# Optimization experiments

Measured on AMD Instinct MI355X. Metric: run time of the kernel, lower is better.

The kernel has to match this reference:

```python
import jax, jax.numpy as jnp
import numpy as np

N = 10000      # nodes
E = 160000     # edges (before self-loops)
H = 8          # heads
D_IN, D_H1, D_H2 = 165, 128, 1    # per-head channels of gat1 / gat2
HID = H * D_H1                    # 1024


def batchnorm(x, gamma, beta, eps=1e-5):
    # training-mode BatchNorm1d: biased batch statistics over the node axis
    mu = x.mean(0)
    var = x.var(0)
    return (x - mu) * jax.lax.rsqrt(var + eps) * gamma + beta


def gatv2(x, src, dst, Wl, bl, Wr, br, att, bias, heads, out_ch, concat, n_nodes):
    # PyG GATv2Conv: lin_l on source, lin_r on target; e = att . LeakyReLU(xl_j + xr_i)
    xl = (x @ Wl + bl).reshape(n_nodes, heads, out_ch)   # source transform
    xr = (x @ Wr + br).reshape(n_nodes, heads, out_ch)   # target transform
    e = jax.nn.leaky_relu(xl[src] + xr[dst], 0.2)        # [E,H,C]
    logits = jnp.einsum('ehc,hc->eh', e, att)            # [E,H]
    # segment softmax over incoming edges of each destination node
    m = jax.lax.stop_gradient(jax.ops.segment_max(logits, dst, num_segments=n_nodes))
    a = jnp.exp(logits - m[dst])
    s = jax.ops.segment_sum(a, dst, num_segments=n_nodes)
    alpha = a / (s[dst] + 1e-16)                          # [E,H]
    out = jax.ops.segment_sum(xl[src] * alpha[..., None], dst, num_segments=n_nodes)
    out = out.reshape(n_nodes, heads * out_ch) if concat else out.mean(1)
    return out + bias


def setup_inputs() -> dict:
    key = jax.random.key(0)
    ks = jax.random.split(key, 12)
    g = lambda k, shape, fan_in: jax.random.normal(k, shape, jnp.float32) * (1.0 / np.sqrt(fan_in))
    return {
        'x': jax.random.normal(ks[0], (N, D_IN), jnp.float32),
        'gamma1': jnp.ones((D_IN,), jnp.float32),
        'beta1': jnp.zeros((D_IN,), jnp.float32),
        'Wl1': g(ks[1], (D_IN, HID), D_IN),
        'bl1': jnp.zeros((HID,), jnp.float32),
        'Wr1': g(ks[2], (D_IN, HID), D_IN),
        'br1': jnp.zeros((HID,), jnp.float32),
        'att1': g(ks[3], (H, D_H1), D_H1),
        'bias1': jnp.zeros((HID,), jnp.float32),
        'gamma2': jnp.ones((HID,), jnp.float32),
        'beta2': jnp.zeros((HID,), jnp.float32),
        'Wl2': g(ks[4], (HID, H * D_H2), HID),
        'bl2': jnp.zeros((H * D_H2,), jnp.float32),
        'Wr2': g(ks[5], (HID, H * D_H2), HID),
        'br2': jnp.zeros((H * D_H2,), jnp.float32),
        'att2': g(ks[6], (H, D_H2), D_H2),
        'bias2': jnp.zeros((D_H2,), jnp.float32),
        'edge_index': jax.random.randint(ks[7], (2, E), 0, N, jnp.int64 if jax.config.jax_enable_x64 else jnp.int32),
    }


def reference(x, gamma1, beta1, Wl1, bl1, Wr1, br1, att1, bias1,
              gamma2, beta2, Wl2, bl2, Wr2, br2, att2, bias2, edge_index):
    loops = jnp.arange(N, dtype=edge_index.dtype)
    src = jnp.concatenate([edge_index[0], loops])   # add_self_loops=True (PyG default)
    dst = jnp.concatenate([edge_index[1], loops])
    h = batchnorm(x, gamma1, beta1)
    h = gatv2(h, src, dst, Wl1, bl1, Wr1, br1, att1, bias1, H, D_H1, True, N)
    h = batchnorm(h, gamma2, beta2)
    h = jax.nn.leaky_relu(h, 0.01)                  # F.leaky_relu default slope
    out = gatv2(h, src, dst, Wl2, bl2, Wr2, br2, att2, bias2, H, D_H2, False, N)
    return out
```

## Files before the change

kernel.cpp:

```cpp
#include <hip/hip_runtime.h>

#define NN   10000
#define E0   160000
#define ET   170000
#define DIN  165
#define KP   192
#define HID  1024
#define NH   8
#define AP   200
#define CP   136
#define K2P  1032
#define BNROW 64
#define BNBLK 157


typedef __bf16 bf16x8 __attribute__((ext_vector_type(8)));
typedef float  f32x4  __attribute__((ext_vector_type(4)));
typedef float  f32x2  __attribute__((ext_vector_type(2)));

__device__ __forceinline__ float bf2f(unsigned short u) {
    unsigned int i = ((unsigned int)u) << 16;
    return __builtin_bit_cast(float, i);
}
__device__ __forceinline__ unsigned short f2bf(float f) {
    unsigned int i = __builtin_bit_cast(unsigned int, f);
    i += 0x7fffu + ((i >> 16) & 1u);
    return (unsigned short)(i >> 16);
}
__device__ __forceinline__ float fin(float x) {
    return fminf(fmaxf(x, -1e30f), 1e30f);
}
__device__ __forceinline__ int clampi(int s) {
    return min(max(s, 0), NN - 1);
}
__device__ __forceinline__ void unpack8(uint4 u, float* f) {
    f[0]=bf2f((unsigned short)(u.x)); f[1]=bf2f((unsigned short)(u.x>>16));
    f[2]=bf2f((unsigned short)(u.y)); f[3]=bf2f((unsigned short)(u.y>>16));
    f[4]=bf2f((unsigned short)(u.z)); f[5]=bf2f((unsigned short)(u.z>>16));
    f[6]=bf2f((unsigned short)(u.w)); f[7]=bf2f((unsigned short)(u.w>>16));
}
__device__ __forceinline__ f32x2 up2(unsigned int u) {
    f32x2 r;
    r.x = __builtin_bit_cast(float, u << 16);
    r.y = __builtin_bit_cast(float, u & 0xffff0000u);
    return r;
}

__global__ __launch_bounds__(256) void debug_fill(float* __restrict__ out, float val) {
    int i = blockIdx.x * 256 + threadIdx.x;
    if (i < NN) out[i] = val;
}

__global__ __launch_bounds__(256) void fuseA_kernel(const float* __restrict__ x,
                                                    float* __restrict__ colsum, float* __restrict__ colsq,
                                                    const int* __restrict__ ei, int* __restrict__ deg) {
    __shared__ float xs[BNROW * DIN];
    const int b = blockIdx.x;
    const int tid = threadIdx.x;
    if (b < BNBLK) {
        const int r0 = b * BNROW;
        const int nrows = min(BNROW, NN - r0);
        const int total = nrows * DIN;
        const float2* src = (const float2*)(x + (size_t)r0 * DIN);
        float2* dstl = (float2*)xs;
        for (int idx = tid; idx < (total >> 1); idx += 256)
            dstl[idx] = src[idx];
        __syncthreads();
        const int c = tid;
        if (c >= DIN) return;
        float a0=0,a1=0,a2=0,a3=0, q0=0,q1=0,q2=0,q3=0;
        int r = 0;
        for (; r + 3 < nrows; r += 4) {
            float v0 = xs[(r    ) * DIN + c];
            float v1 = xs[(r + 1) * DIN + c];
            float v2 = xs[(r + 2) * DIN + c];
            float v3 = xs[(r + 3) * DIN + c];
            a0 += v0; q0 += v0 * v0;
            a1 += v1; q1 += v1 * v1;
            a2 += v2; q2 += v2 * v2;
            a3 += v3; q3 += v3 * v3;
        }
        for (; r < nrows; ++r) {
            float v = xs[r * DIN + c];
            a0 += v; q0 += v * v;
        }
        atomicAdd(&colsum[c], (a0 + a1) + (a2 + a3));
        atomicAdd(&colsq[c],  (q0 + q1) + (q2 + q3));
    } else {
        int e = (b - BNBLK) * 256 + tid;
        if (e >= ET) return;
        int d = (e < E0) ? ei[E0 + e] : (e - E0);
        atomicAdd(&deg[clampi(d)], 1);
    }
}

__global__ __launch_bounds__(1024) void fuseB_kernel(
    const int* __restrict__ deg,
    int* __restrict__ offs, int* __restrict__ cur, int* __restrict__ perm,
    const float* __restrict__ x,
    const float* __restrict__ colsum, const float* __restrict__ colsq,
    const float* __restrict__ gamma, const float* __restrict__ beta,
    unsigned short* __restrict__ hn) {
    if (blockIdx.x != 0) {
        int idx = (blockIdx.x - 1) * 1024 + threadIdx.x;
        if (idx >= NN * KP) return;
        int r = idx / KP, c = idx - r * KP;
        float v = 0.f;
        if (c < DIN) {
            float mu  = colsum[c] * (1.f / NN);
            float var = fmaxf(colsq[c] * (1.f / NN) - mu * mu, 0.f);
            float a = gamma[c] * rsqrtf(var + 1e-5f);
            float b = beta[c] - mu * a;
            v = fin(x[(size_t)r * DIN + c] * a + b);
        }
        hn[idx] = f2bf(v);
        return;
    }
    __shared__ int wsum[16];
    __shared__ int bins[64];
    __shared__ int bcur[64];
    const int tid = threadIdx.x;
    const int base = tid * 10;
    int loc[10];
    int run = 0;
    #pragma unroll
    for (int j = 0; j < 10; ++j) {
        int idx = base + j;
        int v = (idx < NN) ? deg[idx] : 0;
        loc[j] = run;
        run += v;
    }
    const int lane = tid & 63;
    const int w = tid >> 6;
    int inc = run;
    #pragma unroll
    for (int s = 1; s < 64; s <<= 1) {
        int t = __shfl_up(inc, s);
        if (lane >= s) inc += t;
    }
    if (lane == 63) wsum[w] = inc;
    if (tid < 64) bins[tid] = 0;
    __syncthreads();
    int woff = 0;
    #pragma unroll
    for (int k = 0; k < 16; ++k) woff += (k < w) ? wsum[k] : 0;
    const int toff = woff + inc - run;
    #pragma unroll
    for (int j = 0; j < 10; ++j) {
        int idx = base + j;
        if (idx < NN) {
            int e = toff + loc[j]; offs[idx] = e; cur[idx] = e;
            atomicAdd(&bins[63 - min(deg[idx], 63)], 1);
        }
    }
    if (tid == 1023) offs[NN] = woff + inc;
    __syncthreads();
    if (tid < 64) {
        int v = bins[tid];
        int binc = v;
        #pragma unroll
        for (int s = 1; s < 64; s <<= 1) {
            int t = __shfl_up(binc, s);
            if (tid >= s) binc += t;
        }
        bcur[tid] = binc - v;
    }
    __syncthreads();
    #pragma unroll
    for (int j = 0; j < 10; ++j) {
        int idx = base + j;
        if (idx < NN) {
            int pos = atomicAdd(&bcur[63 - min(deg[idx], 63)], 1);
            perm[pos] = idx;
        }
    }
}

__global__ __launch_bounds__(256) void fuseC_kernel(const float* __restrict__ wl,
                                                    const float* __restrict__ wr,
                                                    unsigned short* __restrict__ wlt,
                                                    unsigned short* __restrict__ wrt,
                                                    const int* __restrict__ ei,
                                                    int* __restrict__ cur, int* __restrict__ ssrc) {
    const int b = blockIdx.x;
    if (b < 192) {
        const int z  = b / 96;
        const int rm = b - z * 96;
        const int ky = rm / 6;
        const int kx = rm - ky * 6;
        const float* src    = z ? wr  : wl;
        unsigned short* dst = z ? wrt : wlt;
        __shared__ float ts[32][65];
        const int k0 = kx * 32;
        const int n0 = ky * 64;
        const int tid = threadIdx.x;
        for (int idx = tid; idx < 32 * 64; idx += 256) {
            int k = idx >> 6, n = idx & 63;
            ts[k][n] = (k0 + k < DIN) ? src[(size_t)(k0 + k) * HID + n0 + n] : 0.f;
        }
        __syncthreads();
        for (int idx = tid; idx < 64 * 32; idx += 256) {
            int n = idx >> 5, k = idx & 31;
            dst[(size_t)(n0 + n) * KP + k0 + k] = f2bf(ts[k][n]);
        }
    } else {
        int e = (b - 192) * 256 + threadIdx.x;
        if (e >= ET) return;
        int s, d;
        if (e < E0) { s = ei[e]; d = ei[E0 + e]; }
        else        { s = e - E0; d = e - E0; }
        int pos = atomicAdd(&cur[clampi(d)], 1);
        if (pos >= 0 && pos < ET) ssrc[pos] = clampi(s);
    }
}

__global__ __launch_bounds__(256) void gemm1_kernel(
    const unsigned short* __restrict__ hn,
    const unsigned short* __restrict__ wlt,
    const unsigned short* __restrict__ wrt,
    const float* __restrict__ bl,
    const float* __restrict__ br,
    unsigned short* __restrict__ xl,
    unsigned short* __restrict__ xr) {
    __shared__ unsigned short as[64 * AP];
    const int tid  = threadIdx.x;
    const int lane = tid & 63;
    const int wave = tid >> 6;
    const int col  = lane & 15;
    const int q    = lane >> 4;

    const int m0 = blockIdx.x * 64;
    const int z  = blockIdx.y >> 3;
    const int nb = (blockIdx.y & 7) * 128;
    const unsigned short* wt = z ? wrt : wlt;

    bf16x8 B[2][6];
    {
        const int bc0 = nb + wave * 32 + col;
        #pragma unroll
        for (int nt = 0; nt < 2; ++nt) {
            const unsigned short* wp = wt + (size_t)(bc0 + nt * 16) * KP + q * 8;
            #pragma unroll
            for (int kt = 0; kt < 6; ++kt)
                B[nt][kt] = __builtin_bit_cast(bf16x8, *(const uint4*)(wp + kt * 32));
        }
    }

    {
        const int r  = tid >> 2;
        const int s0 = (tid & 3) * 48;
        const int grow = m0 + r;
        uint4 t0 = {0,0,0,0}, t1 = t0, t2 = t0, t3 = t0, t4 = t0, t5 = t0;
        if (grow < NN) {
            const unsigned short* gp = hn + (size_t)grow * KP + s0;
            t0 = *(const uint4*)(gp);
            t1 = *(const uint4*)(gp + 8);
            t2 = *(const uint4*)(gp + 16);
            t3 = *(const uint4*)(gp + 24);
            t4 = *(const uint4*)(gp + 32);
            t5 = *(const uint4*)(gp + 40);
        }
        unsigned short* lp = as + r * AP + s0;
        *(uint4*)(lp)      = t0;
        *(uint4*)(lp + 8)  = t1;
        *(uint4*)(lp + 16) = t2;
        *(uint4*)(lp + 24) = t3;
        *(uint4*)(lp + 32) = t4;
        *(uint4*)(lp + 40) = t5;
    }
    __syncthreads();

    f32x4 acc[4][2];
    #pragma unroll
    for (int mi = 0; mi < 4; ++mi)
        for (int nt = 0; nt < 2; ++nt)
            acc[mi][nt][0] = acc[mi][nt][1] = acc[mi][nt][2] = acc[mi][nt][3] = 0.f;

    #pragma unroll
    for (int kt = 0; kt < 6; ++kt) {
        const int kk = kt * 32 + q * 8;
        bf16x8 A[4];
        #pragma unroll
        for (int mi = 0; mi < 4; ++mi)
            A[mi] = __builtin_bit_cast(bf16x8, *(const uint4*)(as + (mi * 16 + col) * AP + kk));
        #pragma unroll
        for (int mi = 0; mi < 4; ++mi) {
            acc[mi][0] = __builtin_amdgcn_mfma_f32_16x16x32_bf16(A[mi], B[0][kt], acc[mi][0], 0, 0, 0);
            acc[mi][1] = __builtin_amdgcn_mfma_f32_16x16x32_bf16(A[mi], B[1][kt], acc[mi][1], 0, 0, 0);
        }
    }

    __syncthreads();
    #pragma unroll
    for (int nt = 0; nt < 2; ++nt) {
        const int lc = wave * 32 + nt * 16 + col;
        const float bv = (z ? br : bl)[nb + lc];
        #pragma unroll
        for (int mi = 0; mi < 4; ++mi) {
            #pragma unroll
            for (int r = 0; r < 4; ++r) {
                const int lr = mi * 16 + q * 4 + r;
                as[lr * CP + lc] = f2bf(fin(acc[mi][nt][r] + bv));
            }
        }
    }
    __syncthreads();
    {
        const int r  = tid >> 2;
        const int sg = (tid & 3) * 32;
        const int grow = m0 + r;
        if (grow < NN) {
            unsigned short* dst = (z ? xr : xl) + (size_t)grow * HID + nb + sg;
            const unsigned short* sp = as + r * CP + sg;
            *(uint4*)(dst)      = *(const uint4*)(sp);
            *(uint4*)(dst + 8)  = *(const uint4*)(sp + 8);
            *(uint4*)(dst + 16) = *(const uint4*)(sp + 16);
            *(uint4*)(dst + 24) = *(const uint4*)(sp + 24);
        }
    }
}

__global__ __launch_bounds__(256) void gat1_node(
    const unsigned short* __restrict__ xl1, const unsigned short* xr1,
    const float* __restrict__ att1, const float* __restrict__ bias1,
    const int* __restrict__ offs, const int* __restrict__ ssrc,
    const int* __restrict__ perm,
    unsigned short* agg) {
    const int lane = threadIdx.x & 63;
    const int wave = threadIdx.x >> 6;
    const int i = perm[blockIdx.x * 4 + wave];
    const int e0 = offs[i];
    const int e1 = max(offs[i + 1], e0);

    f32x2 xr2[8], at2[8], o2[8];
    {
        const uint4* xp = (const uint4*)(xr1 + (size_t)i * HID + lane * 16);
        uint4 u0 = xp[0], u1 = xp[1];
        unsigned int w[8] = {u0.x, u0.y, u0.z, u0.w, u1.x, u1.y, u1.z, u1.w};
        const float4* ap = (const float4*)(att1 + lane * 16);
        float4 a0 = ap[0], a1 = ap[1], a2 = ap[2], a3 = ap[3];
        float af[16] = {a0.x,a0.y,a0.z,a0.w, a1.x,a1.y,a1.z,a1.w,
                        a2.x,a2.y,a2.z,a2.w, a3.x,a3.y,a3.z,a3.w};
        #pragma unroll
        for (int j = 0; j < 8; ++j) {
            xr2[j] = up2(w[j]);
            at2[j].x = af[2*j]; at2[j].y = af[2*j+1];
            o2[j].x = 0.f; o2[j].y = 0.f;
        }
    }
    float s = 0.f;

    int e = e0;
    for (; e + 1 < e1; e += 2) {
        const int s0i = clampi(ssrc[e]);
        const int s1i = clampi(ssrc[e + 1]);
        const uint4* xp0 = (const uint4*)(xl1 + (size_t)s0i * HID + lane * 16);
        const uint4* xp1 = (const uint4*)(xl1 + (size_t)s1i * HID + lane * 16);
        uint4 a0 = xp0[0], a1 = xp0[1], b0 = xp1[0], b1 = xp1[1];
        unsigned int wa[8] = {a0.x,a0.y,a0.z,a0.w, a1.x,a1.y,a1.z,a1.w};
        unsigned int wb[8] = {b0.x,b0.y,b0.z,b0.w, b1.x,b1.y,b1.z,b1.w};
        f32x2 xa[8], xb[8];
        #pragma unroll
        for (int j = 0; j < 8; ++j) { xa[j] = up2(wa[j]); xb[j] = up2(wb[j]); }
        f32x2 pa = {0.f, 0.f}, pb = {0.f, 0.f};
        #pragma unroll
        for (int j = 0; j < 8; ++j) {
            f32x2 va = xa[j] + xr2[j];
            f32x2 vb = xb[j] + xr2[j];
            va = __builtin_elementwise_max(va, 0.2f * va);
            vb = __builtin_elementwise_max(vb, 0.2f * vb);
            pa = __builtin_elementwise_fma(at2[j], va, pa);
            pb = __builtin_elementwise_fma(at2[j], vb, pb);
        }
        float p0 = pa.x + pa.y;
        float p1 = pb.x + pb.y;
        p0 += __shfl_xor(p0, 1); p0 += __shfl_xor(p0, 2); p0 += __shfl_xor(p0, 4);
        p1 += __shfl_xor(p1, 1); p1 += __shfl_xor(p1, 2); p1 += __shfl_xor(p1, 4);
        const float aa0 = __expf(fminf(fin(p0), 50.f));
        const float aa1 = __expf(fminf(fin(p1), 50.f));
        s += aa0 + aa1;
        f32x2 av0; av0.x = aa0; av0.y = aa0;
        f32x2 av1; av1.x = aa1; av1.y = aa1;
        #pragma unroll
        for (int j = 0; j < 8; ++j)
            o2[j] = __builtin_elementwise_fma(av0, xa[j],
                    __builtin_elementwise_fma(av1, xb[j], o2[j]));
    }
    if (e < e1) {
        const int sidx = clampi(ssrc[e]);
        const uint4* xp = (const uint4*)(xl1 + (size_t)sidx * HID + lane * 16);
        uint4 u0 = xp[0], u1 = xp[1];
        unsigned int w[8] = {u0.x,u0.y,u0.z,u0.w, u1.x,u1.y,u1.z,u1.w};
        f32x2 xv[8];
        #pragma unroll
        for (int j = 0; j < 8; ++j) xv[j] = up2(w[j]);
        f32x2 p2 = {0.f, 0.f};
        #pragma unroll
        for (int j = 0; j < 8; ++j) {
            f32x2 v = xv[j] + xr2[j];
            v = __builtin_elementwise_max(v, 0.2f * v);
            p2 = __builtin_elementwise_fma(at2[j], v, p2);
        }
        float p = p2.x + p2.y;
        p += __shfl_xor(p, 1); p += __shfl_xor(p, 2); p += __shfl_xor(p, 4);
        const float a = __expf(fminf(fin(p), 50.f));
        s += a;
        f32x2 av; av.x = a; av.y = a;
        #pragma unroll
        for (int j = 0; j < 8; ++j)
            o2[j] = __builtin_elementwise_fma(av, xv[j], o2[j]);
    }

    const float inv = 1.f / (s + 1e-16f);
    const float4* bp = (const float4*)(bias1 + lane * 16);
    float4 b0 = bp[0], b1 = bp[1], b2 = bp[2], b3 = bp[3];
    float bb[16] = {b0.x,b0.y,b0.z,b0.w, b1.x,b1.y,b1.z,b1.w,
                    b2.x,b2.y,b2.z,b2.w, b3.x,b3.y,b3.z,b3.w};
    unsigned short ov[16];
    #pragma unroll
    for (int j = 0; j < 8; ++j) {
        ov[2*j]   = f2bf(fin(o2[j].x * inv + bb[2*j]));
        ov[2*j+1] = f2bf(fin(o2[j].y * inv + bb[2*j+1]));
    }
    uint4* op = (uint4*)(agg + (size_t)i * HID + lane * 16);
    op[0] = *(const uint4*)&ov[0];
    op[1] = *(const uint4*)&ov[8];
}

__global__ __launch_bounds__(256) void bn2_stats(const unsigned short* __restrict__ agg,
                                                 float* __restrict__ colsum, float* __restrict__ colsq) {
    __shared__ float mrg[128 * 16];
    const int tid  = threadIdx.x;
    const int half = tid >> 7;
    const int cc   = (tid & 127) * 8;
    const int r0   = blockIdx.x * 80 + half;
    float s[8], q[8];
    #pragma unroll
    for (int j = 0; j < 8; ++j) { s[j] = 0.f; q[j] = 0.f; }
    #pragma unroll 4
    for (int rr = 0; rr < 40; ++rr) {
        const int r = r0 + rr * 2;
        uint4 u = *(const uint4*)(agg + (size_t)r * HID + cc);
        float v[8];
        unpack8(u, v);
        #pragma unroll
        for (int j = 0; j < 8; ++j) { s[j] += v[j]; q[j] += v[j] * v[j]; }
    }
    if (half) {
        float* m = &mrg[(tid & 127) * 16];
        #pragma unroll
        for (int j = 0; j < 8; ++j) { m[j] = s[j]; m[8 + j] = q[j]; }
    }
    __syncthreads();
    if (!half) {
        const float* m = &mrg[tid * 16];
        #pragma unroll
        for (int j = 0; j < 8; ++j) {
            atomicAdd(&colsum[cc + j], s[j] + m[j]);
            atomicAdd(&colsq[cc + j],  q[j] + m[8 + j]);
        }
    }
}

__global__ __launch_bounds__(256) void gemm2_kernel(
    const unsigned short* __restrict__ agg,
    const float* __restrict__ colsum, const float* __restrict__ colsq,
    const float* __restrict__ gamma, const float* __restrict__ beta,
    const float* __restrict__ wl2, const float* __restrict__ wr2,
    const float* __restrict__ bl2, const float* __restrict__ br2,
    float* __restrict__ xl2, float* __restrict__ xr2) {
    __shared__ unsigned short bs[16 * K2P];
    __shared__ float a2s[HID], b2s[HID];
    __shared__ float red[4 * 64 * 4];
    const int tid  = threadIdx.x;
    const int lane = tid & 63;
    const int wave = tid >> 6;
    const int col  = lane & 15;
    const int q    = lane >> 4;

    for (int idx = tid; idx < 16 * HID; idx += 256) {
        int n = idx >> 10, k = idx & (HID - 1);
        float v = (n < 8) ? wl2[k * 8 + n] : wr2[k * 8 + (n - 8)];
        bs[n * K2P + k] = f2bf(v);
    }
    for (int cc = tid; cc < HID; cc += 256) {
        float mu  = colsum[cc] * (1.f / NN);
        float var = fmaxf(colsq[cc] * (1.f / NN) - mu * mu, 0.f);
        float a = gamma[cc] * rsqrtf(var + 1e-5f);
        a2s[cc] = a; b2s[cc] = beta[cc] - mu * a;
    }
    __syncthreads();

    const int m0 = blockIdx.x * 16;
    const int am = m0 + col;

    uint4 u[8];
    #pragma unroll
    for (int t = 0; t < 8; ++t) {
        const int kk = (wave * 8 + t) * 32 + q * 8;
        u[t] = *(const uint4*)(agg + (size_t)am * HID + kk);
    }

    f32x4 acc;
    acc[0] = acc[1] = acc[2] = acc[3] = 0.f;
    #pragma unroll
    for (int t = 0; t < 8; ++t) {
        const int kk = (wave * 8 + t) * 32 + q * 8;
        float xv[8];
        unpack8(u[t], xv);
        unsigned short hv[8];
        #pragma unroll
        for (int j = 0; j < 8; ++j) {
            float v = xv[j] * a2s[kk + j] + b2s[kk + j];
            v = fmaxf(v, 0.01f * v);
            hv[j] = f2bf(fin(v));
        }
        bf16x8 af = __builtin_bit_cast(bf16x8, *(const uint4*)hv);
        bf16x8 bf = __builtin_bit_cast(bf16x8, *(const uint4*)&bs[col * K2P + kk]);
        acc = __builtin_amdgcn_mfma_f32_16x16x32_bf16(af, bf, acc, 0, 0, 0);
    }

    *(f32x4*)&red[(wave * 64 + lane) * 4] = acc;
    __syncthreads();
    if (wave == 0) {
        f32x4 a0 = *(const f32x4*)&red[lane * 4];
        f32x4 a1 = *(const f32x4*)&red[(64 + lane) * 4];
        f32x4 a2 = *(const f32x4*)&red[(128 + lane) * 4];
        f32x4 a3 = *(const f32x4*)&red[(192 + lane) * 4];
        acc = (a0 + a1) + (a2 + a3);
        const float bv = (col < 8) ? bl2[col] : br2[col - 8];
        float* outp = (col < 8) ? (xl2 + col) : (xr2 + (col - 8));
        #pragma unroll
        for (int r = 0; r < 4; ++r) {
            const int row = m0 + q * 4 + r;
            outp[row * 8] = fin(acc[r] + bv);
        }
    }
}

__global__ __launch_bounds__(256) void gat2_node(
    const float* __restrict__ xl2, const float* __restrict__ xr2,
    const float* __restrict__ att2, const float* __restrict__ bias2,
    const int* __restrict__ offs, const int* __restrict__ ssrc,
    const int* __restrict__ perm,
    float* __restrict__ out) {
    const int lane = threadIdx.x & 63;
    const int wave = threadIdx.x >> 6;
    const int i = perm[blockIdx.x * 4 + wave];
    const int h = lane & 7, slot = lane >> 3;
    const int e0 = offs[i];
    const int e1 = max(offs[i + 1], e0);
    const float xr_h = xr2[i * 8 + h];
    const float att_h = att2[h];
    float ssum = 0.f, wsum = 0.f;
    for (int eb = e0; eb < e1; eb += 8) {
        int e = eb + slot;
        if (e < e1) {
            float xlv = xl2[clampi(ssrc[e]) * 8 + h];
            float v = xlv + xr_h;
            v = fmaxf(v, 0.2f * v);
            float a = __expf(fminf(fin(att_h * v), 50.f));
            ssum += a; wsum += a * xlv;
        }
    }
    ssum += __shfl_xor(ssum, 8); ssum += __shfl_xor(ssum, 16); ssum += __shfl_xor(ssum, 32);
    wsum += __shfl_xor(wsum, 8); wsum += __shfl_xor(wsum, 16); wsum += __shfl_xor(wsum, 32);
    float v = fin(wsum / (ssum + 1e-16f));
    v += __shfl_xor(v, 1); v += __shfl_xor(v, 2); v += __shfl_xor(v, 4);
    if (lane == 0) out[i] = fin(v * 0.125f + bias2[0]);
}

extern "C" void kernel_launch(void* const* d_in, const int* in_sizes, int n_in,
                              void* d_out, int out_size, void* d_ws, size_t ws_size,
                              hipStream_t stream) {
    float* out = (float*)d_out;

    static const int expected[18] = {
        NN * DIN, DIN, DIN, DIN * HID, HID, DIN * HID, HID, HID, HID,
        HID, HID, HID * NH, NH, HID * NH, NH, NH, 1, 2 * E0
    };
    if (n_in != 18) {
        debug_fill<<<(NN + 255) / 256, 256, 0, stream>>>(out, 8192.f + 64.f * (float)n_in);
        return;
    }
    for (int i = 0; i < 18; ++i) {
        if (in_sizes[i] != expected[i]) {
            debug_fill<<<(NN + 255) / 256, 256, 0, stream>>>(out, 4096.f + 32.f * (float)i);
            return;
        }
    }

    const float* x      = (const float*)d_in[0];
    const float* gamma1 = (const float*)d_in[1];
    const float* beta1  = (const float*)d_in[2];
    const float* Wl1    = (const float*)d_in[3];
    const float* bl1    = (const float*)d_in[4];
    const float* Wr1    = (const float*)d_in[5];
    const float* br1    = (const float*)d_in[6];
    const float* att1   = (const float*)d_in[7];
    const float* bias1  = (const float*)d_in[8];
    const float* gamma2 = (const float*)d_in[9];
    const float* beta2  = (const float*)d_in[10];
    const float* Wl2    = (const float*)d_in[11];
    const float* bl2    = (const float*)d_in[12];
    const float* Wr2    = (const float*)d_in[13];
    const float* br2    = (const float*)d_in[14];
    const float* att2   = (const float*)d_in[15];
    const float* bias2  = (const float*)d_in[16];
    const int*   ei     = (const int*)d_in[17];

    char* p = (char*)d_ws;
    auto alloc = [&](size_t bytes) -> void* {
        void* r = (void*)p;
        p += (bytes + 255) & ~(size_t)255;
        return r;
    };
    unsigned short* xl1  = (unsigned short*)alloc((size_t)NN * HID * 2);
    unsigned short* xr1  = (unsigned short*)alloc((size_t)NN * HID * 2);
    unsigned short* agg  = xr1;
    unsigned short* hn   = (unsigned short*)alloc((size_t)NN * KP * 2);
    unsigned short* wlt  = (unsigned short*)alloc((size_t)HID * KP * 2);
    unsigned short* wrt  = (unsigned short*)alloc((size_t)HID * KP * 2);
    float*          xl2  = (float*)alloc((size_t)NN * 8 * 4);
    float*          xr2  = (float*)alloc((size_t)NN * 8 * 4);
    int*            offs = (int*)alloc((NN + 1) * 4);
    int*            cur  = (int*)alloc(NN * 4);
    int*            ssrc = (int*)alloc(ET * 4);
    int*            perm = (int*)alloc(NN * 4);
    char* zbase = p;
    float* colsum1 = (float*)alloc(DIN * 4);
    float* colsq1  = (float*)alloc(DIN * 4);
    float* colsum2 = (float*)alloc(HID * 4);
    float* colsq2  = (float*)alloc(HID * 4);
    int*   deg     = (int*)alloc(NN * 4);
    size_t zlen = (size_t)(p - zbase);
    hipMemsetAsync(zbase, 0, zlen, stream);

    fuseA_kernel<<<BNBLK + (ET + 255) / 256, 256, 0, stream>>>(x, colsum1, colsq1, ei, deg);
    fuseB_kernel<<<1 + (NN * KP + 1023) / 1024, 1024, 0, stream>>>(
        deg, offs, cur, perm, x, colsum1, colsq1, gamma1, beta1, hn);
    fuseC_kernel<<<192 + (ET + 255) / 256, 256, 0, stream>>>(Wl1, Wr1, wlt, wrt, ei, cur, ssrc);
    gemm1_kernel<<<dim3((NN + 63) / 64, 16), 256, 0, stream>>>(hn, wlt, wrt, bl1, br1, xl1, xr1);
    gat1_node<<<NN / 4, 256, 0, stream>>>(xl1, xr1, att1, bias1, offs, ssrc, perm, agg);
    bn2_stats<<<125, 256, 0, stream>>>(agg, colsum2, colsq2);
    gemm2_kernel<<<NN / 16, 256, 0, stream>>>(agg, colsum2, colsq2, gamma2, beta2,
                                              Wl2, Wr2, bl2, br2, xl2, xr2);
    gat2_node<<<NN / 4, 256, 0, stream>>>(xl2, xr2, att2, bias2, offs, ssrc, perm, out);
}
```

Baseline: 280.8 us.

## Split gat1 aggregation across channel quarters and edge halves per wave

Each destination node's GATv2 aggregation is now spread across four blocks, each handling a 256-channel quarter, and the wave's two 32-lane halves process alternating edges before combining their partial sums with a cross-half shuffle. The grid grows fourfold and each lane holds 8 channels instead of 16. This aims to raise parallelism and occupancy and to shorten the serial edge loop on the dominant gather kernel. The cost is extra index loads and repeated setup across blocks, a wider shuffle reduction, and half-filled lanes at the tail of odd-degree nodes.

```diff
diff --git a/kernel.cpp b/kernel.cpp
--- a/kernel.cpp
+++ b/kernel.cpp
@@ -326,105 +326,78 @@
     const int* __restrict__ offs, const int* __restrict__ ssrc,
     const int* __restrict__ perm,
     unsigned short* agg) {
-    const int lane = threadIdx.x & 63;
-    const int wave = threadIdx.x >> 6;
-    const int i = perm[blockIdx.x * 4 + wave];
+    const int lane    = threadIdx.x & 63;
+    const int wv      = threadIdx.x >> 6;
+    const int quarter = blockIdx.x & 3;
+    const int ngrp    = blockIdx.x >> 2;
+    const int i  = perm[ngrp * 4 + wv];
     const int e0 = offs[i];
-    const int e1 = max(offs[i + 1], e0);
-
-    f32x2 xr2[8], at2[8], o2[8];
+    const int e1 = max(offs[i + 1], e0 + 1);
+    const int cl    = lane & 31;
+    const int halfB = lane >> 5;
+    const int choff = quarter * 256 + cl * 8;
+
+    f32x2 xr2[4], at2[4], o2[4];
     {
-        const uint4* xp = (const uint4*)(xr1 + (size_t)i * HID + lane * 16);
-        uint4 u0 = xp[0], u1 = xp[1];
-        unsigned int w[8] = {u0.x, u0.y, u0.z, u0.w, u1.x, u1.y, u1.z, u1.w};
-        const float4* ap = (const float4*)(att1 + lane * 16);
-        float4 a0 = ap[0], a1 = ap[1], a2 = ap[2], a3 = ap[3];
-        float af[16] = {a0.x,a0.y,a0.z,a0.w, a1.x,a1.y,a1.z,a1.w,
-                        a2.x,a2.y,a2.z,a2.w, a3.x,a3.y,a3.z,a3.w};
-        #pragma unroll
-        for (int j = 0; j < 8; ++j) {
-            xr2[j] = up2(w[j]);
-            at2[j].x = af[2*j]; at2[j].y = af[2*j+1];
-            o2[j].x = 0.f; o2[j].y = 0.f;
-        }
+        uint4 u = *(const uint4*)(xr1 + (size_t)i * HID + choff);
+        xr2[0] = up2(u.x); xr2[1] = up2(u.y); xr2[2] = up2(u.z); xr2[3] = up2(u.w);
+        float4 a0 = *(const float4*)(att1 + choff);
+        float4 a1 = *(const float4*)(att1 + choff + 4);
+        at2[0].x = a0.x; at2[0].y = a0.y; at2[1].x = a0.z; at2[1].y = a0.w;
+        at2[2].x = a1.x; at2[2].y = a1.y; at2[3].x = a1.z; at2[3].y = a1.w;
+        #pragma unroll
+        for (int j = 0; j < 4; ++j) { o2[j].x = 0.f; o2[j].y = 0.f; }
     }
     float s = 0.f;
 
-    int e = e0;
-    for (; e + 1 < e1; e += 2) {
-        const int s0i = clampi(ssrc[e]);
-        const int s1i = clampi(ssrc[e + 1]);
-        const uint4* xp0 = (const uint4*)(xl1 + (size_t)s0i * HID + lane * 16);
-        const uint4* xp1 = (const uint4*)(xl1 + (size_t)s1i * HID + lane * 16);
-        uint4 a0 = xp0[0], a1 = xp0[1], b0 = xp1[0], b1 = xp1[1];
-        unsigned int wa[8] = {a0.x,a0.y,a0.z,a0.w, a1.x,a1.y,a1.z,a1.w};
-        unsigned int wb[8] = {b0.x,b0.y,b0.z,b0.w, b1.x,b1.y,b1.z,b1.w};
-        f32x2 xa[8], xb[8];
-        #pragma unroll
-        for (int j = 0; j < 8; ++j) { xa[j] = up2(wa[j]); xb[j] = up2(wb[j]); }
-        f32x2 pa = {0.f, 0.f}, pb = {0.f, 0.f};
-        #pragma unroll
-        for (int j = 0; j < 8; ++j) {
-            f32x2 va = xa[j] + xr2[j];
-            f32x2 vb = xb[j] + xr2[j];
-            va = __builtin_elementwise_max(va, 0.2f * va);
-            vb = __builtin_elementwise_max(vb, 0.2f * vb);
-            pa = __builtin_elementwise_fma(at2[j], va, pa);
-            pb = __builtin_elementwise_fma(at2[j], vb, pb);
-        }
-        float p0 = pa.x + pa.y;
-        float p1 = pb.x + pb.y;
-        p0 += __shfl_xor(p0, 1); p0 += __shfl_xor(p0, 2); p0 += __shfl_xor(p0, 4);
-        p1 += __shfl_xor(p1, 1); p1 += __shfl_xor(p1, 2); p1 += __shfl_xor(p1, 4);
-        const float aa0 = __expf(fminf(fin(p0), 50.f));
-        const float aa1 = __expf(fminf(fin(p1), 50.f));
-        s += aa0 + aa1;
-        f32x2 av0; av0.x = aa0; av0.y = aa0;
-        f32x2 av1; av1.x = aa1; av1.y = aa1;
-        #pragma unroll
-        for (int j = 0; j < 8; ++j)
-            o2[j] = __builtin_elementwise_fma(av0, xa[j],
-                    __builtin_elementwise_fma(av1, xb[j], o2[j]));
-    }
-    if (e < e1) {
-        const int sidx = clampi(ssrc[e]);
-        const uint4* xp = (const uint4*)(xl1 + (size_t)sidx * HID + lane * 16);
-        uint4 u0 = xp[0], u1 = xp[1];
-        unsigned int w[8] = {u0.x,u0.y,u0.z,u0.w, u1.x,u1.y,u1.z,u1.w};
-        f32x2 xv[8];
-        #pragma unroll
-        for (int j = 0; j < 8; ++j) xv[j] = up2(w[j]);
-        f32x2 p2 = {0.f, 0.f};
-        #pragma unroll
-        for (int j = 0; j < 8; ++j) {
-            f32x2 v = xv[j] + xr2[j];
-            v = __builtin_elementwise_max(v, 0.2f * v);
-            p2 = __builtin_elementwise_fma(at2[j], v, p2);
-        }
-        float p = p2.x + p2.y;
-        p += __shfl_xor(p, 1); p += __shfl_xor(p, 2); p += __shfl_xor(p, 4);
-        const float a = __expf(fminf(fin(p), 50.f));
+    const int trips = (e1 - e0 + 1) >> 1;
+    for (int t = 0; t < trips; ++t) {
+        const int e  = e0 + 2 * t + halfB;
+        const bool ok = (e < e1);
+        const int sidx = clampi(ssrc[min(e, e1 - 1)]);
+        const uint4 u = *(const uint4*)(xl1 + (size_t)sidx * HID + choff);
+        f32x2 x0 = up2(u.x), x1 = up2(u.y), x2 = up2(u.z), x3 = up2(u.w);
+        f32x2 v0 = x0 + xr2[0], v1 = x1 + xr2[1], v2 = x2 + xr2[2], v3 = x3 + xr2[3];
+        v0 = __builtin_elementwise_max(v0, 0.2f * v0);
+        v1 = __builtin_elementwise_max(v1, 0.2f * v1);
+        v2 = __builtin_elementwise_max(v2, 0.2f * v2);
+        v3 = __builtin_elementwise_max(v3, 0.2f * v3);
+        f32x2 p = at2[0] * v0;
+        p = __builtin_elementwise_fma(at2[1], v1, p);
+        p = __builtin_elementwise_fma(at2[2], v2, p);
+        p = __builtin_elementwise_fma(at2[3], v3, p);
+        float r = p.x + p.y;
+        r += __shfl_xor(r, 1); r += __shfl_xor(r, 2);
+        r += __shfl_xor(r, 4); r += __shfl_xor(r, 8);
+        const float a = ok ? __expf(fminf(fin(r), 50.f)) : 0.f;
         s += a;
         f32x2 av; av.x = a; av.y = a;
-        #pragma unroll
-        for (int j = 0; j < 8; ++j)
-            o2[j] = __builtin_elementwise_fma(av, xv[j], o2[j]);
-    }
-
-    const float inv = 1.f / (s + 1e-16f);
-    const float4* bp = (const float4*)(bias1 + lane * 16);
-    float4 b0 = bp[0], b1 = bp[1], b2 = bp[2], b3 = bp[3];
-    float bb[16] = {b0.x,b0.y,b0.z,b0.w, b1.x,b1.y,b1.z,b1.w,
-                    b2.x,b2.y,b2.z,b2.w, b3.x,b3.y,b3.z,b3.w};
-    unsigned short ov[16];
-    #pragma unroll
-    for (int j = 0; j < 8; ++j) {
-        ov[2*j]   = f2bf(fin(o2[j].x * inv + bb[2*j]));
-        ov[2*j+1] = f2bf(fin(o2[j].y * inv + bb[2*j+1]));
-    }
-    uint4* op = (uint4*)(agg + (size_t)i * HID + lane * 16);
-    op[0] = *(const uint4*)&ov[0];
-    op[1] = *(const uint4*)&ov[8];
+        o2[0] = __builtin_elementwise_fma(av, x0, o2[0]);
+        o2[1] = __builtin_elementwise_fma(av, x1, o2[1]);
+        o2[2] = __builtin_elementwise_fma(av, x2, o2[2]);
+        o2[3] = __builtin_elementwise_fma(av, x3, o2[3]);
+    }
+
+    s += __shfl_xor(s, 32);
+    #pragma unroll
+    for (int j = 0; j < 4; ++j) {
+        o2[j].x += __shfl_xor(o2[j].x, 32);
+        o2[j].y += __shfl_xor(o2[j].y, 32);
+    }
+
+    if (halfB == 0) {
+        const float inv = 1.f / (s + 1e-16f);
+        float4 b0 = *(const float4*)(bias1 + choff);
+        float4 b1 = *(const float4*)(bias1 + choff + 4);
+        float bb[8] = {b0.x, b0.y, b0.z, b0.w, b1.x, b1.y, b1.z, b1.w};
+        unsigned short ov[8];
+        #pragma unroll
+        for (int j = 0; j < 4; ++j) {
+            ov[2*j]   = f2bf(fin(o2[j].x * inv + bb[2*j]));
+            ov[2*j+1] = f2bf(fin(o2[j].y * inv + bb[2*j+1]));
+        }
+        *(uint4*)(agg + (size_t)i * HID + choff) = *(const uint4*)ov;
+    }
 }
 
 __global__ __launch_bounds__(256) void bn2_stats(const unsigned short* __restrict__ agg,
@@ -641,7 +614,7 @@
         deg, offs, cur, perm, x, colsum1, colsq1, gamma1, beta1, hn);
     fuseC_kernel<<<192 + (ET + 255) / 256, 256, 0, stream>>>(Wl1, Wr1, wlt, wrt, ei, cur, ssrc);
     gemm1_kernel<<<dim3((NN + 63) / 64, 16), 256, 0, stream>>>(hn, wlt, wrt, bl1, br1, xl1, xr1);
-    gat1_node<<<NN / 4, 256, 0, stream>>>(xl1, xr1, att1, bias1, offs, ssrc, perm, agg);
+    gat1_node<<<NN, 256, 0, stream>>>(xl1, xr1, att1, bias1, offs, ssrc, perm, agg);
     bn2_stats<<<125, 256, 0, stream>>>(agg, colsum2, colsq2);
     gemm2_kernel<<<NN / 16, 256, 0, stream>>>(agg, colsum2, colsq2, gamma2, beta2,
                                               Wl2, Wr2, bl2, br2, xl2, xr2);
```

After: 291.3 us. 1.04x slower.
